# Optimization experiments

Hardware: AMD Instinct MI355X
Metric: run time of the kernel (lower is better)

Reference implementation:

```python
import jax, jax.numpy as jnp
import numpy as np

V = 64                 # |Sigma|
IN_DIM = V + 2         # Sigma + '(' + ')'
OUT_DIM = V + 1        # Sigma + <del>/<end>
H = 512
B = 256
SX = 34                # max proto length 32 + 2 boundaries
SY = 34
BIG_NEG = -1000000000.0


def _one_hot_seq(key, S, batch):
    # '(' at pos 0, L random symbols, ')' at pos L+1, zero padding after
    kl, ks = jax.random.split(key)
    lengths = jax.random.randint(kl, (batch,), 4, S - 1)        # L in [4, S-2]
    syms = jax.random.randint(ks, (S, batch), 0, V)
    pos = jnp.arange(S)[:, None]
    tok = jnp.where(pos == 0, V, jnp.where(pos == lengths[None, :] + 1, V + 1, syms))
    oh = jax.nn.one_hot(tok, IN_DIM, dtype=jnp.float32)
    valid = (pos <= lengths[None, :] + 1).astype(jnp.float32)
    return oh * valid[:, :, None]


def setup_inputs() -> dict:
    key = jax.random.key(0)
    ks = jax.random.split(key, 14)

    def p(k, shape, scale):
        return jax.random.uniform(k, shape, jnp.float32, -scale, scale)

    s = 1.0 / float(np.sqrt(H))
    s2 = 1.0 / float(np.sqrt(2 * H))
    return {
        "sources": _one_hot_seq(ks[0], SX, B),
        "targets": _one_hot_seq(ks[1], SY, B),
        # bidirectional prior LSTM (input IN_DIM -> hidden H, fwd + rev)
        "Wih_f": p(ks[2], (4 * H, IN_DIM), s), "Whh_f": p(ks[3], (4 * H, H), s), "b_f": p(ks[4], (4 * H,), s),
        "Wih_r": p(ks[5], (4 * H, IN_DIM), s), "Whh_r": p(ks[6], (4 * H, H), s), "b_r": p(ks[7], (4 * H,), s),
        # modern LSTM (input IN_DIM -> hidden 2H)
        "Wih_m": p(ks[8], (8 * H, IN_DIM), s2), "Whh_m": p(ks[9], (8 * H, 2 * H), s2), "b_m": p(ks[10], (8 * H,), s2),
        # heads: Linear(2H -> OUT_DIM) + LogSoftmax
        "W_sub": p(ks[11], (OUT_DIM, 2 * H), s2), "b_sub": jnp.zeros((OUT_DIM,), jnp.float32),
        "W_ins": p(ks[12], (OUT_DIM, 2 * H), s2), "b_ins": jnp.zeros((OUT_DIM,), jnp.float32),
    }


def _lstm(x, Wih, Whh, b, hid):
    # torch gate order: i, f, g, o
    bsz = x.shape[1]
    def step(carry, xt):
        h, c = carry
        g = xt @ Wih.T + h @ Whh.T + b
        i, f, gg, o = jnp.split(g, 4, axis=-1)
        c = jax.nn.sigmoid(f) * c + jax.nn.sigmoid(i) * jnp.tanh(gg)
        h = jax.nn.sigmoid(o) * jnp.tanh(c)
        return (h, c), h
    init = (jnp.zeros((bsz, hid), x.dtype), jnp.zeros((bsz, hid), x.dtype))
    _, hs = jax.lax.scan(step, init, x)
    return hs  # [S, B, hid]


def _forward(sources, targets, Wih_f, Whh_f, b_f, Wih_r, Whh_r, b_r,
             Wih_m, Whh_m, b_m, W_sub, b_sub, W_ins, b_ins):
    x_fwd = _lstm(sources, Wih_f, Whh_f, b_f, H)
    x_bwd = _lstm(sources[::-1], Wih_r, Whh_r, b_r, H)[::-1]
    x_emb = jnp.concatenate([x_fwd, x_bwd], axis=-1)   # [SX, B, 2H]
    y_emb = _lstm(targets, Wih_m, Whh_m, b_m, 2 * H)    # [SY, B, 2H]

    # head(x_emb[i] + y_emb[j]) decomposes since Linear is affine
    def pair_logprobs(W, bb):
        lx = jnp.einsum('ibh,oh->ibo', x_emb, W)              # [SX, B, O]
        ly = jnp.einsum('jbh,oh->jbo', y_emb, W) + bb         # [SY, B, O]
        return jax.nn.log_softmax(lx[:, None] + ly[None, :], axis=-1)  # [SX, SY, B, O]

    sub_log = pair_logprobs(W_sub, b_sub)
    ins_log = pair_logprobs(W_ins, b_ins)

    # cell (i, j, b) is computed iff x[i] and y[j] are real (non-padding) one-hots, j <= max_cognat_length
    x_any = sources.sum(-1) > 0                                # [SX, B]
    y_any = targets.sum(-1) > 0                                # [SY, B]
    j_ok = jnp.arange(SY) < SY - 1
    valid = x_any[:, None, :] & (y_any & j_ok[:, None])[None, :, :]   # [SX, SY, B]

    end = jnp.where(valid, ins_log[..., V], BIG_NEG)           # insProbs[V_SIZE]
    dlt = jnp.where(valid, sub_log[..., V], BIG_NEG)           # subProbs[V_SIZE]

    y_next = jnp.pad(targets[1:], ((0, 1), (0, 0), (0, 0)))    # y[j+1], [SY, B, IN_DIM]
    ins_ok = valid & (y_next[..., IN_DIM - 1] == 0)[None]      # not bool(y[j+1, V_SIZE+1])
    ins_val = jnp.einsum('ijbv,jbv->ijb', ins_log[..., :V], y_next[..., :V])
    sub_val = jnp.einsum('ijbv,jbv->ijb', sub_log[..., :V], y_next[..., :V])

    # stacked cached probs: [ins, sub, end, del], each [SX, SY, B]
    return jnp.stack([
        jnp.where(ins_ok, ins_val, BIG_NEG),
        jnp.where(ins_ok, sub_val, BIG_NEG),
        end,
        dlt,
    ])


def reference(sources, targets, Wih_f, Whh_f, b_f, Wih_r, Whh_r, b_r,
              Wih_m, Whh_m, b_m, W_sub, b_sub, W_ins, b_ins):
    return _forward(sources, targets, Wih_f, Whh_f, b_f, Wih_r, Whh_r, b_r,
                    Wih_m, Whh_m, b_m, W_sub, b_sub, W_ins, b_ins)
```

## Files before the change

### kernel.cpp

```cpp
#include <hip/hip_runtime.h>

typedef __attribute__((ext_vector_type(4))) float f32x4;
typedef unsigned char u8;
typedef unsigned long long u64t;

#define BIG_NEG -1000000000.0f

static constexpr int B_  = 256;
static constexpr int SX_ = 34;
static constexpr int SY_ = 34;
static constexpr int IND = 66;
static constexpr int OP_ = 80;

__device__ __forceinline__ f32x4 mfma_fp8(long a, long b, f32x4 c) {
  return __builtin_amdgcn_mfma_f32_16x16x32_fp8_fp8(a, b, c, 0, 0, 0);
}
__device__ __forceinline__ float sigm(float x)  { return 1.0f / (1.0f + __expf(-x)); }
__device__ __forceinline__ float tanhx(float x) { return 2.0f * sigm(2.0f * x) - 1.0f; }
template <bool HI>
__device__ __forceinline__ unsigned pk2(float a, float b, unsigned old) {
  return __builtin_amdgcn_cvt_pk_fp8_f32(a, b, (int)old, HI);
}

__global__ __launch_bounds__(256) void prep_all(
    const float* __restrict__ src, const float* __restrict__ tgt,
    int* __restrict__ tok_x, int* __restrict__ tok_y,
    const float* __restrict__ Wsub, const float* __restrict__ Wins,
    u8* __restrict__ Wcat,
    const float* __restrict__ Wihf, const float* __restrict__ bf,
    const float* __restrict__ Wihr, const float* __restrict__ br,
    const float* __restrict__ Wihm, const float* __restrict__ bm,
    float* __restrict__ Ef, float* __restrict__ Er, float* __restrict__ Em,
    const float* __restrict__ Whf, const float* __restrict__ Whr,
    const float* __restrict__ Whm,
    u8* __restrict__ w8f, u8* __restrict__ w8r, u8* __restrict__ w8m) {
  __shared__ float tile[64 * 67];
  const int blk = blockIdx.x;
  const int tid = threadIdx.x;

  if (blk < 68) {
    int idx = blk * 256 + tid;
    const int half = SX_ * B_;
    const float* base = (idx < half) ? src : tgt;
    int* outp         = (idx < half) ? tok_x : tok_y;
    int k = (idx < half) ? idx : idx - half;
    const float* p = base + (size_t)k * IND;
    int tok = -1;
    for (int v = 0; v < IND; ++v) if (p[v] > 0.5f) tok = v;
    outp[k] = tok;
  } else if (blk < 228) {
    int widx = (blk - 68) * 256 + tid;
    int row = widx >> 8;
    int wc  = widx & 255;
    int srow = row < 80 ? row : row - 80;
    const float* W = row < 80 ? Wsub : Wins;
    float f0 = 0.f, f1 = 0.f, f2 = 0.f, f3 = 0.f;
    if (srow < 65) {
      const float* p = W + (size_t)srow * 1024 + wc * 4;
      f0 = p[0]; f1 = p[1]; f2 = p[2]; f3 = p[3];
    }
    unsigned w = pk2<false>(f0, f1, 0);
    w = pk2<true>(f2, f3, w);
    ((unsigned*)Wcat)[widx] = w;
  } else if (blk < 356) {
    int tb = blk - 228;
    const float* W; const float* bias; float* E; int H4; int n0;
    if (tb < 32)      { W = Wihf; bias = bf; E = Ef; H4 = 2048; n0 = tb * 64; }
    else if (tb < 64) { W = Wihr; bias = br; E = Er; H4 = 2048; n0 = (tb - 32) * 64; }
    else              { W = Wihm; bias = bm; E = Em; H4 = 4096; n0 = (tb - 64) * 64; }
    const float* s2 = W + (size_t)n0 * IND;
    for (int i = tid; i < 64 * IND; i += 256) {
      int n = i / IND, v = i - n * IND;
      tile[n * 67 + v] = s2[i];
    }
    __syncthreads();
    int lane = tid & 63, w2 = tid >> 6;
    float bl = bias[n0 + lane];
    for (int v = w2; v < 67; v += 4) {
      float val = (v < 66 ? tile[lane * 67 + v] : 0.f) + bl;
      E[(size_t)v * H4 + n0 + lane] = val;
    }
  } else {
    const int F4 = 2048 * 512 / 4;
    const int M4 = 4096 * 1024 / 4;
    int i = (blk - 356) * 256 + tid;
    int stride = 3072 * 256;
    for (; i < 2 * F4 + M4; i += stride) {
      const float* s3; unsigned* dst; int k;
      if (i < F4)          { s3 = Whf; dst = (unsigned*)w8f; k = i; }
      else if (i < 2 * F4) { s3 = Whr; dst = (unsigned*)w8r; k = i - F4; }
      else                 { s3 = Whm; dst = (unsigned*)w8m; k = i - 2 * F4; }
      float4 f = ((const float4*)s3)[k];
      unsigned w3 = pk2<false>(f.x, f.y, 0);
      w3 = pk2<true>(f.z, f.w, w3);
      dst[k] = w3;
    }
  }
}

template <int HH, int NS>
__device__ __forceinline__ void run_lstm(
    const u8* __restrict__ w8, const float* __restrict__ E,
    bool revr, u8* __restrict__ hall, int b0, int h0,
    unsigned* __restrict__ flags, int dom0, int myid,
    u8* __restrict__ alds, u8* __restrict__ hT, const u8* __restrict__ tok_small) {
  const int tid = threadIdx.x;
  const int lane = tid & 63, w = tid >> 6;
  const int lo = lane & 15, q = lane >> 4;
  constexpr int AST = HH + 8;
  constexpr int U8C = HH / 8;
  constexpr int USH = (HH == 1024) ? 7 : 6;
  constexpr int NI  = (32 * U8C) / 256;
  constexpr int NK  = HH / 32;
  const int hh = lo & 7;
  const bool hi = (lo >= 8);
  const int hu_e = h0 + w * 8 + hh;

  long breg0[NK], breg1[NK];
  {
    const u8* brow0 = w8 + (size_t)((lo >> 3) * HH + hu_e) * HH + q * 8;
    const u8* brow1 = w8 + (size_t)((2 + (lo >> 3)) * HH + hu_e) * HH + q * 8;
#pragma unroll
    for (int kk = 0; kk < NK; ++kk) {
      breg0[kk] = *(const long*)(brow0 + kk * 32);
      breg1[kk] = *(const long*)(brow1 + kk * 32);
    }
  }
  float creg[4] = {0.f, 0.f, 0.f, 0.f};

  for (int t = 0; t < 34; ++t) {
    f32x4 acc[2][2];
#pragma unroll
    for (int mt = 0; mt < 2; ++mt) {
      acc[mt][0] = (f32x4){0.f, 0.f, 0.f, 0.f};
      acc[mt][1] = (f32x4){0.f, 0.f, 0.f, 0.f};
    }

    if (t > 0) {
      const u8* hsrc = hall + (size_t)t * (256 * HH);
      u64t tmp[NI];
#pragma unroll
      for (int ii = 0; ii < NI; ++ii) {
        int idx = tid + ii * 256;
        tmp[ii] = __hip_atomic_load(
            (const u64t*)(hsrc + (size_t)(b0 + (idx >> USH)) * HH + (idx & (U8C - 1)) * 8),
            __ATOMIC_RELAXED, __HIP_MEMORY_SCOPE_AGENT);
      }
#pragma unroll
      for (int ii = 0; ii < NI; ++ii) {
        int idx = tid + ii * 256;
        *(u64t*)&alds[(idx >> USH) * AST + (idx & (U8C - 1)) * 8] = tmp[ii];
      }
      __syncthreads();

      const u8* a0p = alds + lo * AST + q * 8;
      const u8* a1p = alds + (16 + lo) * AST + q * 8;
#pragma unroll
      for (int kk = 0; kk < NK; ++kk) {
        long a0 = *(const long*)(a0p + kk * 32);
        long a1 = *(const long*)(a1p + kk * 32);
        acc[0][0] = mfma_fp8(a0, breg0[kk], acc[0][0]);
        acc[0][1] = mfma_fp8(a0, breg1[kk], acc[0][1]);
        acc[1][0] = mfma_fp8(a1, breg0[kk], acc[1][0]);
        acc[1][1] = mfma_fp8(a1, breg1[kk], acc[1][1]);
      }
    }

    int tpos = revr ? 33 - t : t;
    const u8* tkp = tok_small + tpos * 32;
#pragma unroll
    for (int mt = 0; mt < 2; ++mt) {
      f32x4 t0 = acc[mt][0], t1 = acc[mt][1];
      f32x4 p0, p1;
#pragma unroll
      for (int c2 = 0; c2 < 4; ++c2) {
        p0[c2] = __shfl_xor(t0[c2], 8, 64);
        p1[c2] = __shfl_xor(t1[c2], 8, 64);
      }
#pragma unroll
      for (int rr = 0; rr < 2; ++rr) {
        int r = (hi ? 2 : 0) + rr;
        float iv = hi ? p0[r] : t0[r];
        float fv = hi ? t0[r] : p0[r];
        float gv = hi ? p1[r] : t1[r];
        float ov = hi ? t1[r] : p1[r];
        int m = mt * 16 + q * 4 + r;
        int v = tkp[m];
        const float* e = E + (size_t)v * (4 * HH) + hu_e;
        iv += e[0]; fv += e[HH]; gv += e[2 * HH]; ov += e[3 * HH];
        float cold = creg[mt * 2 + rr];
        float cn = sigm(fv) * cold + sigm(iv) * tanhx(gv);
        float hn = sigm(ov) * tanhx(cn);
        creg[mt * 2 + rr] = cn;
        hT[m * 32 + w * 8 + hh] = (u8)(pk2<false>(hn, hn, 0) & 0xffu);
      }
    }
    __syncthreads();

    {
      int m = tid >> 3, cc = tid & 7;
      unsigned val = *(const unsigned*)&hT[m * 32 + cc * 4];
      u8* hdst = hall + (size_t)(t + 1) * (256 * HH);
      __hip_atomic_store((unsigned*)(hdst + (size_t)(b0 + m) * HH + h0 + cc * 4),
                         val, __ATOMIC_RELAXED, __HIP_MEMORY_SCOPE_AGENT);
    }

    if (t < 33) {
      __asm__ volatile("s_waitcnt vmcnt(0)" ::: "memory");
      __syncthreads();
      unsigned tgt = (unsigned)(t + 1);
      if (tid == 0)
        __hip_atomic_store(&flags[(dom0 + myid) * 32], tgt,
                           __ATOMIC_RELAXED, __HIP_MEMORY_SCOPE_AGENT);
      if (tid < NS) {
        int spin = 0;
        for (;;) {
          unsigned v = __hip_atomic_load(&flags[(dom0 + tid) * 32],
                                         __ATOMIC_RELAXED, __HIP_MEMORY_SCOPE_AGENT);
          if (__ballot(v < tgt) == 0) break;
          __builtin_amdgcn_s_sleep(1);
          if (++spin > (1 << 17)) break;
        }
      }
      __syncthreads();
    }
  }
}

__global__ __launch_bounds__(256, 2) void lstm_persist(
    const int* __restrict__ tok_x, const int* __restrict__ tok_y,
    const float* __restrict__ E_f, const u8* __restrict__ w8_f,
    const float* __restrict__ E_r, const u8* __restrict__ w8_r,
    const float* __restrict__ E_m, const u8* __restrict__ w8_m,
    u8* __restrict__ fwd_all, u8* __restrict__ rev_all, u8* __restrict__ y_all,
    unsigned* __restrict__ flags) {
  __shared__ u8 alds[32 * 1032];
  __shared__ u8 hT[32 * 32];
  __shared__ u8 tok_small[34 * 32];

  const int b = blockIdx.x;
  int role, c, s;
  if (b < 256)      { role = 2; c = b >> 5; s = b & 31; }
  else if (b < 384) { int l = b - 256; role = 0; c = l >> 4; s = l & 15; }
  else              { int l = b - 384; role = 1; c = l >> 4; s = l & 15; }

  const float* E  = role == 0 ? E_f  : role == 1 ? E_r  : E_m;
  const u8*    w8 = role == 0 ? w8_f : role == 1 ? w8_r : w8_m;
  u8* hall        = role == 0 ? fwd_all : role == 1 ? rev_all : y_all;
  const int* tokg = (role == 2) ? tok_y : tok_x;
  const int b0 = c * 32;
  const int h0 = s * 32;
  const int dom0 = (role == 2) ? c * 32 : (role == 0) ? 256 + c * 16 : 384 + c * 16;

  for (int i = threadIdx.x; i < 34 * 32; i += 256) {
    int t2 = i >> 5, m = i & 31;
    int tk = tokg[t2 * 256 + b0 + m];
    tok_small[i] = (u8)(tk < 0 ? 66 : tk);
  }
  __syncthreads();

  if (role == 2)
    run_lstm<1024, 32>(w8, E, false, hall, b0, h0, flags, dom0, s, alds, hT, tok_small);
  else
    run_lstm<512, 16>(w8, E, role == 1, hall, b0, h0, flags, dom0, s, alds, hT, tok_small);
}

__global__ __launch_bounds__(256, 1) void head_kernel(
    const u8* __restrict__ fwd_all, const u8* __restrict__ rev_all,
    const u8* __restrict__ y_all, const u8* __restrict__ Wcat,
    const float* __restrict__ b_sub, const float* __restrict__ b_ins,
    float* __restrict__ lx_sub, float* __restrict__ lx_ins,
    float* __restrict__ ly_sub, float* __restrict__ ly_ins) {
  __shared__ u8 wq[160 * 264];
  const int lane = threadIdx.x & 63, wave = threadIdx.x >> 6;
  const int lo = lane & 15, q = lane >> 4;
  int blk = blockIdx.x;
  bool yside = (blk >= 136);
  int mb = yside ? blk - 136 : blk;
  int ij = mb >> 2;
  int bbase = (mb & 3) * 64;

  f32x4 acc[10];
#pragma unroll
  for (int nn = 0; nn < 10; ++nn) acc[nn] = (f32x4){0.f,0.f,0.f,0.f};

  for (int qk = 0; qk < 4; ++qk) {
    long aA[8];
    {
      int row = bbase + wave * 16 + lo;
      const u8* ab;
      if (yside)
        ab = y_all + ((size_t)(ij + 1) * 256 + row) * 1024 + qk * 256 + q * 8;
      else if (qk < 2)
        ab = fwd_all + ((size_t)(ij + 1) * 256 + row) * 512 + qk * 256 + q * 8;
      else
        ab = rev_all + ((size_t)(34 - ij) * 256 + row) * 512 + (qk - 2) * 256 + q * 8;
#pragma unroll
      for (int ki = 0; ki < 8; ++ki) aA[ki] = *(const long*)(ab + ki * 32);
    }

    for (int c8 = threadIdx.x; c8 < 160 * 32; c8 += 256) {
      int row = c8 >> 5, col = (c8 & 31) << 3;
      *(long*)&wq[row * 264 + col] =
          *(const long*)&Wcat[(size_t)row * 1024 + qk * 256 + col];
    }
    __syncthreads();

#pragma unroll
    for (int ki = 0; ki < 8; ++ki) {
#pragma unroll
      for (int nn = 0; nn < 10; ++nn) {
        long bf = *(const long*)&wq[(nn * 16 + lo) * 264 + ki * 32 + q * 8];
        acc[nn] = mfma_fp8(aA[ki], bf, acc[nn]);
      }
    }
    __syncthreads();
  }

#pragma unroll
  for (int nn = 0; nn < 10; ++nn) {
    bool is_sub = (nn < 5);
    int n = (is_sub ? nn : nn - 5) * 16 + lo;
    float bias = 0.0f;
    if (yside && n < 65) bias = is_sub ? b_sub[n] : b_ins[n];
    float* dst = yside ? (is_sub ? ly_sub : ly_ins) : (is_sub ? lx_sub : lx_ins);
#pragma unroll
    for (int r = 0; r < 4; ++r) {
      int b = bbase + wave * 16 + q * 4 + r;
      dst[((size_t)ij * 256 + b) * OP_ + n] = acc[nn][r] + bias;
    }
  }
}

__device__ __forceinline__ void lse_one(const float4* __restrict__ X,
                                        const float* __restrict__ py, int sym,
                                        float& logZ, float& v64, float& vs) {
  float v[68];
  const float4* py4 = (const float4*)py;
#pragma unroll
  for (int q = 0; q < 17; ++q) {
    float4 yb = py4[q];
    v[4 * q + 0] = X[q].x + yb.x;
    v[4 * q + 1] = X[q].y + yb.y;
    v[4 * q + 2] = X[q].z + yb.z;
    v[4 * q + 3] = X[q].w + yb.w;
  }
  float m = v[0];
#pragma unroll
  for (int o = 1; o < 65; ++o) m = fmaxf(m, v[o]);
  float s = 0.0f, vsl = 0.0f;
#pragma unroll
  for (int o = 0; o < 65; ++o) {
    s += __expf(v[o] - m);
    if (o < 64) vsl = (o == sym) ? v[o] : vsl;
  }
  logZ = m + __logf(s);
  v64 = v[64];
  vs = vsl;
}

__global__ __launch_bounds__(256, 1) void pair_kernel(
    const int* __restrict__ tok_x, const int* __restrict__ tok_y,
    const float* __restrict__ lx_sub, const float* __restrict__ lx_ins,
    const float* __restrict__ ly_sub, const float* __restrict__ ly_ins,
    float* __restrict__ out) {
  const int hsel = blockIdx.x >= 136;
  const int rem = hsel ? blockIdx.x - 136 : blockIdx.x;
  const int i = rem >> 2;
  const int bc = rem & 3;
  const int jq = threadIdx.x >> 6;
  const int bl = threadIdx.x & 63;
  const int b = bc * 64 + bl;
  const size_t CH = (size_t)SX_ * SY_ * B_;
  const float* lx = hsel ? lx_ins : lx_sub;
  const float* ly = hsel ? ly_ins : ly_sub;
  float* outA = out + (hsel ? 0 : CH);
  float* outB = out + (hsel ? 2 * CH : 3 * CH);

  float4 X[17];
  {
    const float4* ps = (const float4*)(lx + ((size_t)i * 256 + b) * OP_);
#pragma unroll
    for (int q = 0; q < 17; ++q) X[q] = ps[q];
  }
  int tx = tok_x[i * 256 + b];

  for (int j = jq; j < 34; j += 4) {
    size_t obase = ((size_t)i * SY_ + j) * 256 + b;
    bool dead = (j == SY_ - 1) || (tx < 0);
    if (!dead) {
      int ty = tok_y[j * 256 + b];
      if (ty < 0) dead = true;
    }
    if (dead) {
      outA[obase] = BIG_NEG;
      outB[obase] = BIG_NEG;
      continue;
    }
    int tn = tok_y[(j + 1) * 256 + b];
    bool ins_ok = (tn != 65);
    int sym = (tn >= 0 && tn < 64) ? tn : -1;

    float logZ, v64, vs;
    lse_one(X, ly + ((size_t)j * 256 + b) * OP_, sym, logZ, v64, vs);
    float valB = v64 - logZ;
    float valA = (sym >= 0) ? (vs - logZ) : 0.0f;
    outA[obase] = ins_ok ? valA : BIG_NEG;
    outB[obase] = valB;
  }
}

extern "C" void kernel_launch(void* const* d_in, const int* in_sizes, int n_in,
                              void* d_out, int out_size, void* d_ws, size_t ws_size,
                              hipStream_t stream) {
  const float* sources = (const float*)d_in[0];
  const float* targets = (const float*)d_in[1];
  const float* Wih_f = (const float*)d_in[2];
  const float* Whh_f = (const float*)d_in[3];
  const float* b_f   = (const float*)d_in[4];
  const float* Wih_r = (const float*)d_in[5];
  const float* Whh_r = (const float*)d_in[6];
  const float* b_r   = (const float*)d_in[7];
  const float* Wih_m = (const float*)d_in[8];
  const float* Whh_m = (const float*)d_in[9];
  const float* b_m   = (const float*)d_in[10];
  const float* W_sub = (const float*)d_in[11];
  const float* b_sub = (const float*)d_in[12];
  const float* W_ins = (const float*)d_in[13];
  const float* b_ins = (const float*)d_in[14];
  float* out = (float*)d_out;

  char* w = (char*)d_ws;
  constexpr size_t FLAG_SZ = 512 * 32 * 4;
  constexpr size_t TOK_SZ  = (size_t)SX_ * B_ * 4;
  constexpr size_t WCAT_SZ = (size_t)160 * 1024;
  constexpr size_t W8F_SZ  = (size_t)2048 * 512;
  constexpr size_t W8M_SZ  = (size_t)4096 * 1024;
  constexpr size_t EF_SZ   = (size_t)67 * 2048 * 4;
  constexpr size_t EM_SZ   = (size_t)67 * 4096 * 4;
  constexpr size_t LX_SZ   = (size_t)SX_ * B_ * OP_ * 4;
  constexpr size_t HF_SZ   = (size_t)35 * B_ * 512;
  constexpr size_t HM_SZ   = (size_t)35 * B_ * 1024;

  size_t off = 0;
  unsigned* flags = (unsigned*)(w + off); off += FLAG_SZ;
  int*  tok_x   = (int*)(w + off);  off += TOK_SZ;
  int*  tok_y   = (int*)(w + off);  off += TOK_SZ;
  off = (off + 255) & ~(size_t)255;
  u8*   Wcat    = (u8*)(w + off);   off += WCAT_SZ;
  u8*   w8_f    = (u8*)(w + off);   off += W8F_SZ;
  u8*   w8_r    = (u8*)(w + off);   off += W8F_SZ;
  u8*   w8_m    = (u8*)(w + off);   off += W8M_SZ;
  float* E_f    = (float*)(w + off); off += EF_SZ;
  float* E_r    = (float*)(w + off); off += EF_SZ;
  float* E_m    = (float*)(w + off); off += EM_SZ;
  float* lx_sub = (float*)(w + off); off += LX_SZ;
  float* lx_ins = (float*)(w + off); off += LX_SZ;
  float* ly_sub = (float*)(w + off); off += LX_SZ;
  float* ly_ins = (float*)(w + off); off += LX_SZ;
  u8* fwd_all   = (u8*)(w + off);   off += HF_SZ;
  u8* rev_all   = (u8*)(w + off);   off += HF_SZ;
  u8* y_all     = (u8*)(w + off);   off += HM_SZ;
  (void)ws_size; (void)in_sizes; (void)n_in; (void)out_size;

  (void)hipMemsetAsync(flags, 0, FLAG_SZ, stream);

  prep_all<<<3428, 256, 0, stream>>>(
      sources, targets, tok_x, tok_y,
      W_sub, W_ins, Wcat,
      Wih_f, b_f, Wih_r, b_r, Wih_m, b_m, E_f, E_r, E_m,
      Whh_f, Whh_r, Whh_m, w8_f, w8_r, w8_m);

  lstm_persist<<<512, 256, 0, stream>>>(
      tok_x, tok_y,
      E_f, w8_f,
      E_r, w8_r,
      E_m, w8_m,
      fwd_all, rev_all, y_all, flags);

  head_kernel<<<272, 256, 0, stream>>>(fwd_all, rev_all, y_all, Wcat,
                                       b_sub, b_ins, lx_sub, lx_ins, ly_sub, ly_ins);

  pair_kernel<<<272, 256, 0, stream>>>(tok_x, tok_y, lx_sub, lx_ins,
                                       ly_sub, ly_ins, out);
}
```

Baseline: 339.3 us.

## Fuse prep, LSTM and head kernels into one persistent kernel with grid barriers

Merges the weight/embedding prep, the persistent LSTM, and the head GEMM into one 512-block persistent kernel. Global flag-based grid barriers separate the phases, and each phase reuses one shared-memory buffer. The aim is to remove two kernel launches and their gaps. The cost is that the prep work now runs on only 512 blocks instead of 3428, and two full-grid spin barriers are added. It also relies on all 512 blocks being co-resident, with atomic relaxed stores used for the cross-block visibility.

```diff
diff --git a/kernel.cpp b/kernel.cpp
--- a/kernel.cpp
+++ b/kernel.cpp
@@ -21,93 +21,23 @@
 __device__ __forceinline__ unsigned pk2(float a, float b, unsigned old) {
   return __builtin_amdgcn_cvt_pk_fp8_f32(a, b, (int)old, HI);
 }
-
-__global__ __launch_bounds__(256) void prep_all(
-    const float* __restrict__ src, const float* __restrict__ tgt,
-    int* __restrict__ tok_x, int* __restrict__ tok_y,
-    const float* __restrict__ Wsub, const float* __restrict__ Wins,
-    u8* __restrict__ Wcat,
-    const float* __restrict__ Wihf, const float* __restrict__ bf,
-    const float* __restrict__ Wihr, const float* __restrict__ br,
-    const float* __restrict__ Wihm, const float* __restrict__ bm,
-    float* __restrict__ Ef, float* __restrict__ Er, float* __restrict__ Em,
-    const float* __restrict__ Whf, const float* __restrict__ Whr,
-    const float* __restrict__ Whm,
-    u8* __restrict__ w8f, u8* __restrict__ w8r, u8* __restrict__ w8m) {
-  __shared__ float tile[64 * 67];
-  const int blk = blockIdx.x;
-  const int tid = threadIdx.x;
-
-  if (blk < 68) {
-    int idx = blk * 256 + tid;
-    const int half = SX_ * B_;
-    const float* base = (idx < half) ? src : tgt;
-    int* outp         = (idx < half) ? tok_x : tok_y;
-    int k = (idx < half) ? idx : idx - half;
-    const float* p = base + (size_t)k * IND;
-    int tok = -1;
-    for (int v = 0; v < IND; ++v) if (p[v] > 0.5f) tok = v;
-    outp[k] = tok;
-  } else if (blk < 228) {
-    int widx = (blk - 68) * 256 + tid;
-    int row = widx >> 8;
-    int wc  = widx & 255;
-    int srow = row < 80 ? row : row - 80;
-    const float* W = row < 80 ? Wsub : Wins;
-    float f0 = 0.f, f1 = 0.f, f2 = 0.f, f3 = 0.f;
-    if (srow < 65) {
-      const float* p = W + (size_t)srow * 1024 + wc * 4;
-      f0 = p[0]; f1 = p[1]; f2 = p[2]; f3 = p[3];
-    }
-    unsigned w = pk2<false>(f0, f1, 0);
-    w = pk2<true>(f2, f3, w);
-    ((unsigned*)Wcat)[widx] = w;
-  } else if (blk < 356) {
-    int tb = blk - 228;
-    const float* W; const float* bias; float* E; int H4; int n0;
-    if (tb < 32)      { W = Wihf; bias = bf; E = Ef; H4 = 2048; n0 = tb * 64; }
-    else if (tb < 64) { W = Wihr; bias = br; E = Er; H4 = 2048; n0 = (tb - 32) * 64; }
-    else              { W = Wihm; bias = bm; E = Em; H4 = 4096; n0 = (tb - 64) * 64; }
-    const float* s2 = W + (size_t)n0 * IND;
-    for (int i = tid; i < 64 * IND; i += 256) {
-      int n = i / IND, v = i - n * IND;
-      tile[n * 67 + v] = s2[i];
-    }
-    __syncthreads();
-    int lane = tid & 63, w2 = tid >> 6;
-    float bl = bias[n0 + lane];
-    for (int v = w2; v < 67; v += 4) {
-      float val = (v < 66 ? tile[lane * 67 + v] : 0.f) + bl;
-      E[(size_t)v * H4 + n0 + lane] = val;
-    }
-  } else {
-    const int F4 = 2048 * 512 / 4;
-    const int M4 = 4096 * 1024 / 4;
-    int i = (blk - 356) * 256 + tid;
-    int stride = 3072 * 256;
-    for (; i < 2 * F4 + M4; i += stride) {
-      const float* s3; unsigned* dst; int k;
-      if (i < F4)          { s3 = Whf; dst = (unsigned*)w8f; k = i; }
-      else if (i < 2 * F4) { s3 = Whr; dst = (unsigned*)w8r; k = i - F4; }
-      else                 { s3 = Whm; dst = (unsigned*)w8m; k = i - 2 * F4; }
-      float4 f = ((const float4*)s3)[k];
-      unsigned w3 = pk2<false>(f.x, f.y, 0);
-      w3 = pk2<true>(f.z, f.w, w3);
-      dst[k] = w3;
-    }
-  }
+__device__ __forceinline__ void ast32(unsigned* p, unsigned v) {
+  __hip_atomic_store(p, v, __ATOMIC_RELAXED, __HIP_MEMORY_SCOPE_AGENT);
+}
+__device__ __forceinline__ unsigned ald32(const unsigned* p) {
+  return __hip_atomic_load(p, __ATOMIC_RELAXED, __HIP_MEMORY_SCOPE_AGENT);
 }
 
 template <int HH, int NS>
 __device__ __forceinline__ void run_lstm(
     const u8* __restrict__ w8, const float* __restrict__ E,
     bool revr, u8* __restrict__ hall, int b0, int h0,
-    unsigned* __restrict__ flags, int dom0, int myid,
+    unsigned* __restrict__ dom_flags, int myid,
     u8* __restrict__ alds, u8* __restrict__ hT, const u8* __restrict__ tok_small) {
   const int tid = threadIdx.x;
   const int lane = tid & 63, w = tid >> 6;
   const int lo = lane & 15, q = lane >> 4;
-  constexpr int AST = HH + 8;
+  constexpr int AST2 = HH + 8;
   constexpr int U8C = HH / 8;
   constexpr int USH = (HH == 1024) ? 7 : 6;
   constexpr int NI  = (32 * U8C) / 256;
@@ -149,12 +79,12 @@
 #pragma unroll
       for (int ii = 0; ii < NI; ++ii) {
         int idx = tid + ii * 256;
-        *(u64t*)&alds[(idx >> USH) * AST + (idx & (U8C - 1)) * 8] = tmp[ii];
+        *(u64t*)&alds[(idx >> USH) * AST2 + (idx & (U8C - 1)) * 8] = tmp[ii];
       }
       __syncthreads();
 
-      const u8* a0p = alds + lo * AST + q * 8;
-      const u8* a1p = alds + (16 + lo) * AST + q * 8;
+      const u8* a0p = alds + lo * AST2 + q * 8;
+      const u8* a1p = alds + (16 + lo) * AST2 + q * 8;
 #pragma unroll
       for (int kk = 0; kk < NK; ++kk) {
         long a0 = *(const long*)(a0p + kk * 32);
@@ -201,22 +131,18 @@
       int m = tid >> 3, cc = tid & 7;
       unsigned val = *(const unsigned*)&hT[m * 32 + cc * 4];
       u8* hdst = hall + (size_t)(t + 1) * (256 * HH);
-      __hip_atomic_store((unsigned*)(hdst + (size_t)(b0 + m) * HH + h0 + cc * 4),
-                         val, __ATOMIC_RELAXED, __HIP_MEMORY_SCOPE_AGENT);
+      ast32((unsigned*)(hdst + (size_t)(b0 + m) * HH + h0 + cc * 4), val);
     }
 
     if (t < 33) {
       __asm__ volatile("s_waitcnt vmcnt(0)" ::: "memory");
       __syncthreads();
       unsigned tgt = (unsigned)(t + 1);
-      if (tid == 0)
-        __hip_atomic_store(&flags[(dom0 + myid) * 32], tgt,
-                           __ATOMIC_RELAXED, __HIP_MEMORY_SCOPE_AGENT);
+      if (tid == 0) ast32(&dom_flags[myid * 32], tgt);
       if (tid < NS) {
         int spin = 0;
         for (;;) {
-          unsigned v = __hip_atomic_load(&flags[(dom0 + tid) * 32],
-                                         __ATOMIC_RELAXED, __HIP_MEMORY_SCOPE_AGENT);
+          unsigned v = ald32(&dom_flags[tid * 32]);
           if (__ballot(v < tgt) == 0) break;
           __builtin_amdgcn_s_sleep(1);
           if (++spin > (1 << 17)) break;
@@ -227,23 +153,112 @@
   }
 }
 
-__global__ __launch_bounds__(256, 2) void lstm_persist(
-    const int* __restrict__ tok_x, const int* __restrict__ tok_y,
-    const float* __restrict__ E_f, const u8* __restrict__ w8_f,
-    const float* __restrict__ E_r, const u8* __restrict__ w8_r,
-    const float* __restrict__ E_m, const u8* __restrict__ w8_m,
+__global__ __launch_bounds__(256, 2) void mega_kernel(
+    const float* __restrict__ sources, const float* __restrict__ targets,
+    const float* __restrict__ Wih_f, const float* __restrict__ Whh_f, const float* __restrict__ b_f,
+    const float* __restrict__ Wih_r, const float* __restrict__ Whh_r, const float* __restrict__ b_r,
+    const float* __restrict__ Wih_m, const float* __restrict__ Whh_m, const float* __restrict__ b_m,
+    const float* __restrict__ W_sub, const float* __restrict__ b_sub,
+    const float* __restrict__ W_ins, const float* __restrict__ b_ins,
+    int* __restrict__ tok_x, int* __restrict__ tok_y,
+    u8* __restrict__ Wcat, u8* __restrict__ w8_f, u8* __restrict__ w8_r, u8* __restrict__ w8_m,
+    float* __restrict__ E_f, float* __restrict__ E_r, float* __restrict__ E_m,
     u8* __restrict__ fwd_all, u8* __restrict__ rev_all, u8* __restrict__ y_all,
+    float* __restrict__ lx_sub, float* __restrict__ lx_ins,
+    float* __restrict__ ly_sub, float* __restrict__ ly_ins,
     unsigned* __restrict__ flags) {
-  __shared__ u8 alds[32 * 1032];
-  __shared__ u8 hT[32 * 32];
-  __shared__ u8 tok_small[34 * 32];
-
-  const int b = blockIdx.x;
+  __shared__ u8 smem[43520];
+  const int blk = blockIdx.x;
+  const int tid = threadIdx.x;
+
+  if (blk < 68) {
+    int idx = blk * 256 + tid;
+    const int half = SX_ * B_;
+    const float* base = (idx < half) ? sources : targets;
+    int* outp         = (idx < half) ? tok_x : tok_y;
+    int k = (idx < half) ? idx : idx - half;
+    const float* p = base + (size_t)k * IND;
+    int tok = -1;
+    for (int v = 0; v < IND; ++v) if (p[v] > 0.5f) tok = v;
+    ast32((unsigned*)&outp[k], (unsigned)tok);
+  } else if (blk < 228) {
+    int widx = (blk - 68) * 256 + tid;
+    int row = widx >> 8;
+    int wc  = widx & 255;
+    int srow = row < 80 ? row : row - 80;
+    const float* W = row < 80 ? W_sub : W_ins;
+    float f0 = 0.f, f1 = 0.f, f2 = 0.f, f3 = 0.f;
+    if (srow < 65) {
+      const float* p = W + (size_t)srow * 1024 + wc * 4;
+      f0 = p[0]; f1 = p[1]; f2 = p[2]; f3 = p[3];
+    }
+    unsigned w = pk2<false>(f0, f1, 0);
+    w = pk2<true>(f2, f3, w);
+    ast32(&((unsigned*)Wcat)[widx], w);
+  } else if (blk < 356) {
+    float* tile = (float*)smem;
+    int tb = blk - 228;
+    const float* W; const float* bias; float* E; int H4; int n0;
+    if (tb < 32)      { W = Wih_f; bias = b_f; E = E_f; H4 = 2048; n0 = tb * 64; }
+    else if (tb < 64) { W = Wih_r; bias = b_r; E = E_r; H4 = 2048; n0 = (tb - 32) * 64; }
+    else              { W = Wih_m; bias = b_m; E = E_m; H4 = 4096; n0 = (tb - 64) * 64; }
+    const float* s2 = W + (size_t)n0 * IND;
+    for (int i = tid; i < 64 * IND; i += 256) {
+      int n = i / IND, v = i - n * IND;
+      tile[n * 67 + v] = s2[i];
+    }
+    __syncthreads();
+    int lane = tid & 63, w2 = tid >> 6;
+    float bl = bias[n0 + lane];
+    for (int v = w2; v < 67; v += 4) {
+      float val = (v < 66 ? tile[lane * 67 + v] : 0.f) + bl;
+      ast32((unsigned*)&E[(size_t)v * H4 + n0 + lane], __float_as_uint(val));
+    }
+    __syncthreads();
+  }
+  {
+    const int F4 = 2048 * 512 / 4;
+    const int M4 = 4096 * 1024 / 4;
+    int i = blk * 256 + tid;
+    const int stride = 512 * 256;
+    for (; i < 2 * F4 + M4; i += stride) {
+      const float* s3; unsigned* dst; int k;
+      if (i < F4)          { s3 = Whh_f; dst = (unsigned*)w8_f; k = i; }
+      else if (i < 2 * F4) { s3 = Whh_r; dst = (unsigned*)w8_r; k = i - F4; }
+      else                 { s3 = Whh_m; dst = (unsigned*)w8_m; k = i - 2 * F4; }
+      float4 f = ((const float4*)s3)[k];
+      unsigned w3 = pk2<false>(f.x, f.y, 0);
+      w3 = pk2<true>(f.z, f.w, w3);
+      ast32(&dst[k], w3);
+    }
+  }
+
+  {
+    __asm__ volatile("s_waitcnt vmcnt(0)" ::: "memory");
+    __syncthreads();
+    if (tid == 0) ast32(&flags[blk * 32], 1u);
+    if (tid < 64) {
+      int spin = 0;
+      for (;;) {
+        bool bad = false;
+        for (int k = tid; k < 512; k += 64)
+          if (ald32(&flags[k * 32]) < 1u) { bad = true; break; }
+        if (__ballot(bad) == 0) break;
+        __builtin_amdgcn_s_sleep(2);
+        if (++spin > (1 << 17)) break;
+      }
+    }
+    __syncthreads();
+    __asm__ volatile("" ::: "memory");
+  }
+
   int role, c, s;
-  if (b < 256)      { role = 2; c = b >> 5; s = b & 31; }
-  else if (b < 384) { int l = b - 256; role = 0; c = l >> 4; s = l & 15; }
-  else              { int l = b - 384; role = 1; c = l >> 4; s = l & 15; }
-
+  {
+    const int b = blk;
+    if (b < 256)      { role = 2; c = b >> 5; s = b & 31; }
+    else if (b < 384) { int l = b - 256; role = 0; c = l >> 4; s = l & 15; }
+    else              { int l = b - 384; role = 1; c = l >> 4; s = l & 15; }
+  }
   const float* E  = role == 0 ? E_f  : role == 1 ? E_r  : E_m;
   const u8*    w8 = role == 0 ? w8_f : role == 1 ? w8_r : w8_m;
   u8* hall        = role == 0 ? fwd_all : role == 1 ? rev_all : y_all;
@@ -251,8 +266,14 @@
   const int b0 = c * 32;
   const int h0 = s * 32;
   const int dom0 = (role == 2) ? c * 32 : (role == 0) ? 256 + c * 16 : 384 + c * 16;
-
-  for (int i = threadIdx.x; i < 34 * 32; i += 256) {
+  unsigned* lf = flags + 512 * 32;
+  unsigned* dom_flags = lf + dom0 * 32;
+
+  u8* alds = smem;
+  u8* hT = smem + 33024;
+  u8* tok_small = smem + 34048;
+
+  for (int i = tid; i < 34 * 32; i += 256) {
     int t2 = i >> 5, m = i & 31;
     int tk = tokg[t2 * 256 + b0 + m];
     tok_small[i] = (u8)(tk < 0 ? 66 : tk);
@@ -260,74 +281,87 @@
   __syncthreads();
 
   if (role == 2)
-    run_lstm<1024, 32>(w8, E, false, hall, b0, h0, flags, dom0, s, alds, hT, tok_small);
+    run_lstm<1024, 32>(w8, E, false, hall, b0, h0, dom_flags, s, alds, hT, tok_small);
   else
-    run_lstm<512, 16>(w8, E, role == 1, hall, b0, h0, flags, dom0, s, alds, hT, tok_small);
-}
-
-__global__ __launch_bounds__(256, 1) void head_kernel(
-    const u8* __restrict__ fwd_all, const u8* __restrict__ rev_all,
-    const u8* __restrict__ y_all, const u8* __restrict__ Wcat,
-    const float* __restrict__ b_sub, const float* __restrict__ b_ins,
-    float* __restrict__ lx_sub, float* __restrict__ lx_ins,
-    float* __restrict__ ly_sub, float* __restrict__ ly_ins) {
-  __shared__ u8 wq[160 * 264];
-  const int lane = threadIdx.x & 63, wave = threadIdx.x >> 6;
-  const int lo = lane & 15, q = lane >> 4;
-  int blk = blockIdx.x;
-  bool yside = (blk >= 136);
-  int mb = yside ? blk - 136 : blk;
-  int ij = mb >> 2;
-  int bbase = (mb & 3) * 64;
-
-  f32x4 acc[10];
-#pragma unroll
-  for (int nn = 0; nn < 10; ++nn) acc[nn] = (f32x4){0.f,0.f,0.f,0.f};
-
-  for (int qk = 0; qk < 4; ++qk) {
-    long aA[8];
-    {
-      int row = bbase + wave * 16 + lo;
-      const u8* ab;
-      if (yside)
-        ab = y_all + ((size_t)(ij + 1) * 256 + row) * 1024 + qk * 256 + q * 8;
-      else if (qk < 2)
-        ab = fwd_all + ((size_t)(ij + 1) * 256 + row) * 512 + qk * 256 + q * 8;
-      else
-        ab = rev_all + ((size_t)(34 - ij) * 256 + row) * 512 + (qk - 2) * 256 + q * 8;
-#pragma unroll
-      for (int ki = 0; ki < 8; ++ki) aA[ki] = *(const long*)(ab + ki * 32);
-    }
-
-    for (int c8 = threadIdx.x; c8 < 160 * 32; c8 += 256) {
-      int row = c8 >> 5, col = (c8 & 31) << 3;
-      *(long*)&wq[row * 264 + col] =
-          *(const long*)&Wcat[(size_t)row * 1024 + qk * 256 + col];
-    }
-    __syncthreads();
-
-#pragma unroll
-    for (int ki = 0; ki < 8; ++ki) {
-#pragma unroll
-      for (int nn = 0; nn < 10; ++nn) {
-        long bf = *(const long*)&wq[(nn * 16 + lo) * 264 + ki * 32 + q * 8];
-        acc[nn] = mfma_fp8(aA[ki], bf, acc[nn]);
-      }
-    }
-    __syncthreads();
-  }
-
-#pragma unroll
-  for (int nn = 0; nn < 10; ++nn) {
-    bool is_sub = (nn < 5);
-    int n = (is_sub ? nn : nn - 5) * 16 + lo;
-    float bias = 0.0f;
-    if (yside && n < 65) bias = is_sub ? b_sub[n] : b_ins[n];
-    float* dst = yside ? (is_sub ? ly_sub : ly_ins) : (is_sub ? lx_sub : lx_ins);
-#pragma unroll
-    for (int r = 0; r < 4; ++r) {
-      int b = bbase + wave * 16 + q * 4 + r;
-      dst[((size_t)ij * 256 + b) * OP_ + n] = acc[nn][r] + bias;
+    run_lstm<512, 16>(w8, E, role == 1, hall, b0, h0, dom_flags, s, alds, hT, tok_small);
+
+  {
+    __asm__ volatile("s_waitcnt vmcnt(0)" ::: "memory");
+    __syncthreads();
+    if (tid == 0) ast32(&lf[(dom0 + s) * 32], 34u);
+    if (tid < 64) {
+      int spin = 0;
+      for (;;) {
+        bool bad = false;
+        for (int k = tid; k < 512; k += 64)
+          if (ald32(&lf[k * 32]) < 34u) { bad = true; break; }
+        if (__ballot(bad) == 0) break;
+        __builtin_amdgcn_s_sleep(2);
+        if (++spin > (1 << 17)) break;
+      }
+    }
+    __syncthreads();
+    __asm__ volatile("" ::: "memory");
+  }
+
+  if (blk >= 272) return;
+  {
+    u8* wq = smem;
+    const int lane = tid & 63, wave = tid >> 6;
+    const int lo = lane & 15, q = lane >> 4;
+    bool yside = (blk >= 136);
+    int mb = yside ? blk - 136 : blk;
+    int ij = mb >> 2;
+    int bbase = (mb & 3) * 64;
+
+    f32x4 acc[10];
+#pragma unroll
+    for (int nn = 0; nn < 10; ++nn) acc[nn] = (f32x4){0.f,0.f,0.f,0.f};
+
+    for (int qk = 0; qk < 4; ++qk) {
+      long aA[8];
+      {
+        int row = bbase + wave * 16 + lo;
+        const u8* ab;
+        if (yside)
+          ab = y_all + ((size_t)(ij + 1) * 256 + row) * 1024 + qk * 256 + q * 8;
+        else if (qk < 2)
+          ab = fwd_all + ((size_t)(ij + 1) * 256 + row) * 512 + qk * 256 + q * 8;
+        else
+          ab = rev_all + ((size_t)(34 - ij) * 256 + row) * 512 + (qk - 2) * 256 + q * 8;
+#pragma unroll
+        for (int ki = 0; ki < 8; ++ki) aA[ki] = *(const long*)(ab + ki * 32);
+      }
+      __syncthreads();
+      for (int c8 = tid; c8 < 160 * 32; c8 += 256) {
+        int row = c8 >> 5, col = (c8 & 31) << 3;
+        *(long*)&wq[row * 264 + col] =
+            *(const long*)&Wcat[(size_t)row * 1024 + qk * 256 + col];
+      }
+      __syncthreads();
+
+#pragma unroll
+      for (int ki = 0; ki < 8; ++ki) {
+#pragma unroll
+        for (int nn = 0; nn < 10; ++nn) {
+          long bf = *(const long*)&wq[(nn * 16 + lo) * 264 + ki * 32 + q * 8];
+          acc[nn] = mfma_fp8(aA[ki], bf, acc[nn]);
+        }
+      }
+    }
+
+#pragma unroll
+    for (int nn = 0; nn < 10; ++nn) {
+      bool is_sub = (nn < 5);
+      int n = (is_sub ? nn : nn - 5) * 16 + lo;
+      float bias = 0.0f;
+      if (yside && n < 65) bias = is_sub ? b_sub[n] : b_ins[n];
+      float* dst = yside ? (is_sub ? ly_sub : ly_ins) : (is_sub ? lx_sub : lx_ins);
+#pragma unroll
+      for (int r = 0; r < 4; ++r) {
+        int b = bbase + wave * 16 + q * 4 + r;
+        dst[((size_t)ij * 256 + b) * OP_ + n] = acc[nn][r] + bias;
+      }
     }
   }
 }
@@ -431,7 +465,7 @@
   float* out = (float*)d_out;
 
   char* w = (char*)d_ws;
-  constexpr size_t FLAG_SZ = 512 * 32 * 4;
+  constexpr size_t FLAG_SZ = 1024 * 32 * 4;
   constexpr size_t TOK_SZ  = (size_t)SX_ * B_ * 4;
   constexpr size_t WCAT_SZ = (size_t)160 * 1024;
   constexpr size_t W8F_SZ  = (size_t)2048 * 512;
@@ -465,21 +499,18 @@
 
   (void)hipMemsetAsync(flags, 0, FLAG_SZ, stream);
 
-  prep_all<<<3428, 256, 0, stream>>>(
-      sources, targets, tok_x, tok_y,
-      W_sub, W_ins, Wcat,
-      Wih_f, b_f, Wih_r, b_r, Wih_m, b_m, E_f, E_r, E_m,
-      Whh_f, Whh_r, Whh_m, w8_f, w8_r, w8_m);
-
-  lstm_persist<<<512, 256, 0, stream>>>(
+  mega_kernel<<<512, 256, 0, stream>>>(
+      sources, targets,
+      Wih_f, Whh_f, b_f,
+      Wih_r, Whh_r, b_r,
+      Wih_m, Whh_m, b_m,
+      W_sub, b_sub, W_ins, b_ins,
       tok_x, tok_y,
-      E_f, w8_f,
-      E_r, w8_r,
-      E_m, w8_m,
-      fwd_all, rev_all, y_all, flags);
-
-  head_kernel<<<272, 256, 0, stream>>>(fwd_all, rev_all, y_all, Wcat,
-                                       b_sub, b_ins, lx_sub, lx_ins, ly_sub, ly_ins);
+      Wcat, w8_f, w8_r, w8_m,
+      E_f, E_r, E_m,
+      fwd_all, rev_all, y_all,
+      lx_sub, lx_ins, ly_sub, ly_ins,
+      flags);
 
   pair_kernel<<<272, 256, 0, stream>>>(tok_x, tok_y, lx_sub, lx_ins,
                                        ly_sub, ly_ins, out);
```

Result: slower. 347.9 us (+2.5%).
